# Kernel optimization log

Measured on AMD Instinct MI355X. Metric: run time of the kernel, lower is better.

## Reference

```python
import jax, jax.numpy as jnp
import numpy as np

N_NODES = 10000
DIM = 512
HEADS = 8
HEAD_DIM = DIM // HEADS  # 64
TOPK = 6
EPS = 1e-5
SLOPE = 0.01  # torch LeakyReLU default


def _layernorm(x, w, b):
    mu = x.mean(axis=-1, keepdims=True)
    var = ((x - mu) ** 2).mean(axis=-1, keepdims=True)
    return (x - mu) / jnp.sqrt(var + EPS) * w + b


def setup_inputs() -> dict:
    key = jax.random.key(0)
    ks = jax.random.split(key, 8)

    def w(k, shape):
        return jax.random.normal(k, shape, dtype=jnp.float32) * 0.02

    return {
        "x": jax.random.normal(ks[0], (1, N_NODES, DIM), dtype=jnp.float32),
        "fc1_w": w(ks[1], (DIM, DIM)), "fc1_b": jnp.zeros((DIM,), jnp.float32),
        "wh_w": w(ks[2], (DIM, DIM)), "wh_b": jnp.zeros((DIM,), jnp.float32),
        "wt_w": w(ks[3], (DIM, DIM)), "wt_b": jnp.zeros((DIM,), jnp.float32),
        "q_w": w(ks[4], (DIM, DIM)), "q_b": jnp.zeros((DIM,), jnp.float32),
        "kv_w": w(ks[5], (2 * DIM, DIM)), "kv_b": jnp.zeros((2 * DIM,), jnp.float32),
        "lin_w": w(ks[6], (DIM, DIM)), "lin_b": jnp.zeros((DIM,), jnp.float32),
        "norm_w": jnp.ones((DIM,), jnp.float32),
        "norm_b": jnp.zeros((DIM,), jnp.float32),
    }


def reference(x, fc1_w, fc1_b, wh_w, wh_b, wt_w, wt_b, q_w, q_b,
              kv_w, kv_b, lin_w, lin_b, norm_w, norm_b):
    # x: [1, N, DIM]
    n = x.shape[1]
    scale = HEAD_DIM ** -0.5

    x_input = x
    h = jax.nn.leaky_relu(x @ fc1_w.T + fc1_b, SLOPE)
    h = (h + h.mean(axis=1, keepdims=True)) * 0.5

    e_h = h @ wh_w.T + wh_b            # [1, N, DIM]
    e_t = h @ wt_w.T + wt_b            # [1, N, DIM]

    # dense graph-construction scores + per-row top-k neighbors
    logits = (e_h * scale) @ jnp.swapaxes(e_t, -2, -1)   # [1, N, N]
    _, topk_idx = jax.lax.top_k(logits, TOPK)            # [1, N, TOPK]

    # prototype node = most frequent tail index (torch unique+counts+argsort, top=1)
    counts = jnp.bincount(topk_idx.reshape(-1), length=n)
    top_node = jnp.argmax(counts)

    ins_top = jnp.take(x_input, top_node[None], axis=1)  # [1, 1, DIM]
    q_feat = jnp.take(h, top_node[None], axis=1)[0, 0]   # [DIM]

    # gather k=TOPK neighbor tail embeddings per node
    nb = e_t[0][topk_idx[0]]                              # [N, TOPK, DIM]

    q_heads = (q_feat @ q_w.T + q_b).reshape(HEADS, HEAD_DIM) * scale
    kv = (nb @ kv_w.T + kv_b).reshape(n, TOPK, 2, HEADS, HEAD_DIM)
    k_, v_ = kv[:, :, 0], kv[:, :, 1]                     # [N, TOPK, H, HD]

    attn = jnp.einsum('hd,nehd->nhe', q_heads, k_)        # [N, H, TOPK]
    attn = jax.nn.softmax(attn, axis=-1)
    out = jnp.einsum('nhe,nehd->nhd', attn, v_).reshape(n, DIM)

    e_nh = _layernorm(out, norm_w, norm_b)[None]          # [1, N, DIM]

    s = _layernorm(e_h + e_nh, norm_w, norm_b)
    s = jax.nn.leaky_relu(s @ lin_w.T + lin_b, SLOPE)     # dropout = identity (eval)
    embedding = s + x_input
    return embedding, ins_top
```

## Files before the change

kernel.cpp:

```cpp
#include <hip/hip_runtime.h>
#include <hip/hip_bf16.h>
#include <math.h>

#define N_NODES 10000
#define DIM 512
#define TOPK 6
#define NCHUNK 10
#define CHUNK 1024
#define NL 4
#define NCK 8
#define NC2 16
#define SLOPE 0.01
#define LN_EPS 1e-5f

typedef short bf16x8 __attribute__((ext_vector_type(8)));
typedef float f32x4 __attribute__((ext_vector_type(4)));
typedef double f64x4 __attribute__((ext_vector_type(4)));

__device__ __forceinline__ unsigned pack_key(float v, int idx)
{
    unsigned b = __float_as_uint(v);
    unsigned m = b ^ ((unsigned)((int)b >> 31) | 0x80000000u);
    return (m & 0xFFFFC000u) | (16383u - (unsigned)idx);
}

template <int D>
__device__ __forceinline__ void insert_u(unsigned (&k)[D], unsigned nk)
{
    if (nk > k[D - 1]) {
        k[D - 1] = nk;
#pragma unroll
        for (int s = D - 1; s > 0; s--) {
            unsigned hi = max(k[s], k[s - 1]);
            unsigned lo = min(k[s], k[s - 1]);
            k[s - 1] = hi; k[s] = lo;
        }
    }
}

__device__ __forceinline__ void gload16(const void* g, void* l)
{
    __builtin_amdgcn_global_load_lds(
        (const __attribute__((address_space(1))) void*)g,
        (__attribute__((address_space(3))) void*)l, 16, 0, 0);
}

__global__ __launch_bounds__(256) void colsum_part64(
    const double* __restrict__ h, double* __restrict__ part, int n, int nb)
{
    int b = blockIdx.x;
    int rows_per = (n + nb - 1) / nb;
    int r0 = b * rows_per, r1 = min(n, r0 + rows_per);
    int t = threadIdx.x;
    double s0 = 0.0, s1 = 0.0;
    for (int i = r0; i < r1; i++) {
        s0 += h[(size_t)i * DIM + t];
        s1 += h[(size_t)i * DIM + t + 256];
    }
    part[b * DIM + t] = s0;
    part[b * DIM + t + 256] = s1;
}

__global__ void colmean64(const double* __restrict__ part, double* __restrict__ mean,
                          int nb, int n)
{
    int j = blockIdx.x * blockDim.x + threadIdx.x;
    if (j < DIM) {
        double s = 0.0;
        for (int b = 0; b < nb; b++) s += part[b * DIM + j];
        mean[j] = s / (double)n;
    }
}

__global__ void cast_wb(const float* __restrict__ in1, short* __restrict__ o1, int n1,
                        const float* __restrict__ in2, short* __restrict__ o2)
{
    int i = (blockIdx.x * blockDim.x + threadIdx.x) * 4;
    const float* in = (i < n1) ? in1 + i : in2 + (i - n1);
    short* o = (i < n1) ? o1 + i : o2 + (i - n1);
    float4 f = *(const float4*)in;
    __hip_bfloat16 b0 = __float2bfloat16(f.x), b1 = __float2bfloat16(f.y);
    __hip_bfloat16 b2 = __float2bfloat16(f.z), b3 = __float2bfloat16(f.w);
    *(short4*)o = make_short4(*(short*)&b0, *(short*)&b1, *(short*)&b2, *(short*)&b3);
}

template <int POST, bool AF32, bool MIX, bool CASTF, bool CASTB>
__global__ __launch_bounds__(256, 4) void mfma_gemm_f64(
    const void* __restrict__ Av, const float* __restrict__ W,
    const float* __restrict__ bias, const double* __restrict__ mn,
    double* __restrict__ C, float* __restrict__ of, short* __restrict__ ob,
    int n, int K, int M)
{
    __shared__ double As[64][18];
    __shared__ double Bs[128][18];
    const int t = threadIdx.x, lane = t & 63, wid = t >> 6;
    const int lx = lane & 15, q = lane >> 4;
    const int wr = (wid >> 1) * 32, wc = (wid & 1) * 64;
    const int i0 = blockIdx.x * 64, j0 = blockIdx.y * 128;

    f64x4 acc[2][4];
#pragma unroll
    for (int a = 0; a < 2; a++)
#pragma unroll
        for (int b = 0; b < 4; b++) acc[a][b] = (f64x4)0.0;

    const int arow = t >> 2, askq = (t & 3) * 4;
    int gi = i0 + arow; if (gi >= n) gi = n - 1;
    const float*  af32 = (const float*)Av + (size_t)gi * K + askq;
    const double* af64 = (const double*)Av + (size_t)gi * K + askq;
    const int brow = t >> 1, bskq = (t & 1) * 8;
    const float* wrow = W + (size_t)(j0 + brow) * K + bskq;

    float4 wv0 = *(const float4*)(wrow);
    float4 wv1 = *(const float4*)(wrow + 4);
    float4 av;
    double2 a0v, a1v;
    if (AF32) av = *(const float4*)(af32);
    else { a0v = *(const double2*)(af64); a1v = *(const double2*)(af64 + 2); }

    for (int k0 = 0; k0 < K; k0 += 16) {
        __syncthreads();
        double m0 = 0, m1 = 0, m2 = 0, m3 = 0;
        if (MIX) {
            double2 mv0 = *(const double2*)(mn + k0 + askq);
            double2 mv1 = *(const double2*)(mn + k0 + askq + 2);
            m0 = mv0.x; m1 = mv0.y; m2 = mv1.x; m3 = mv1.y;
        }
        if (AF32) {
            As[arow][askq]     = (double)av.x; As[arow][askq + 1] = (double)av.y;
            As[arow][askq + 2] = (double)av.z; As[arow][askq + 3] = (double)av.w;
        } else if (MIX) {
            As[arow][askq]     = (a0v.x + m0) * 0.5; As[arow][askq + 1] = (a0v.y + m1) * 0.5;
            As[arow][askq + 2] = (a1v.x + m2) * 0.5; As[arow][askq + 3] = (a1v.y + m3) * 0.5;
        } else {
            As[arow][askq]     = a0v.x; As[arow][askq + 1] = a0v.y;
            As[arow][askq + 2] = a1v.x; As[arow][askq + 3] = a1v.y;
        }
        Bs[brow][bskq]     = (double)wv0.x; Bs[brow][bskq + 1] = (double)wv0.y;
        Bs[brow][bskq + 2] = (double)wv0.z; Bs[brow][bskq + 3] = (double)wv0.w;
        Bs[brow][bskq + 4] = (double)wv1.x; Bs[brow][bskq + 5] = (double)wv1.y;
        Bs[brow][bskq + 6] = (double)wv1.z; Bs[brow][bskq + 7] = (double)wv1.w;
        if (k0 + 16 < K) {
            wv0 = *(const float4*)(wrow + k0 + 16);
            wv1 = *(const float4*)(wrow + k0 + 20);
            if (AF32) av = *(const float4*)(af32 + k0 + 16);
            else { a0v = *(const double2*)(af64 + k0 + 16);
                   a1v = *(const double2*)(af64 + k0 + 18); }
        }
        __syncthreads();

#pragma unroll
        for (int ks = 0; ks < 4; ks++) {
            double a0 = As[wr + lx][ks * 4 + q];
            double a1 = As[wr + 16 + lx][ks * 4 + q];
#pragma unroll
            for (int cf = 0; cf < 4; cf++) {
                double b = Bs[wc + cf * 16 + lx][ks * 4 + q];
                acc[0][cf] = __builtin_amdgcn_mfma_f64_16x16x4f64(a0, b, acc[0][cf], 0, 0, 0);
                acc[1][cf] = __builtin_amdgcn_mfma_f64_16x16x4f64(a1, b, acc[1][cf], 0, 0, 0);
            }
        }
    }

#pragma unroll
    for (int rf = 0; rf < 2; rf++)
#pragma unroll
        for (int cf = 0; cf < 4; cf++)
#pragma unroll
            for (int reg = 0; reg < 4; reg++) {
                int gi2 = i0 + wr + rf * 16 + q * 4 + reg;
                int gj2 = j0 + wc + cf * 16 + lx;
                if (gi2 < n) {
                    double v = acc[rf][cf][reg] + (double)bias[gj2];
                    if (POST == 1) v = (v >= 0.0) ? v : v * SLOPE;
                    size_t idx = (size_t)gi2 * M + gj2;
                    C[idx] = v;
                    if (CASTF || CASTB) {
                        float f = (float)v;
                        if (CASTF) of[idx] = f;
                        if (CASTB) {
                            __hip_bfloat16 bb = __float2bfloat16(f);
                            ob[idx] = *reinterpret_cast<short*>(&bb);
                        }
                    }
                }
            }
}

__global__ __launch_bounds__(256, 3) void logits_topk_mfma(
    const short* __restrict__ eh, const short* __restrict__ et,
    unsigned* __restrict__ pk, int n)
{
    __shared__ short As[2][4096];
    __shared__ short Bs[2][4096];
    const int t = threadIdx.x;
    const int lane = t & 63, wid = t >> 6;
    const int lx = lane & 15, q = lane >> 4;

    int id = blockIdx.x, bx, chunk;
    if (id < 632) { chunk = id & 7; bx = id >> 3; }
    else { int r = id - 632; chunk = 8 + (r & 1); bx = r >> 1; }
    const int i0 = bx * 128;
    const int wbase = wid * 32;

    const int jlo = chunk * CHUNK;
    const int jhi = min(n, jlo + CHUNK);
    const int nj = (jhi - jlo + 127) >> 7;
    const int np = nj * 16;

    const int sslot = (t & 3) ^ ((t >> 3) & 3);
    const short* aP[2];
    const short* bP[2];
#pragma unroll
    for (int is = 0; is < 2; is++) {
        int row = is * 64 + (t >> 2);
        int ra = i0 + row; if (ra >= n) ra = n - 1;
        aP[is] = eh + (size_t)ra * DIM + sslot * 8;
    }
    const int slotq = (q ^ ((lx >> 1) & 3)) * 8;
    const int aOff = (wbase + lx) * 32 + slotq;
    const int bOff = lx * 32 + slotq;

    unsigned keys[8][NL];
#pragma unroll
    for (int r = 0; r < 8; r++)
#pragma unroll
        for (int s = 0; s < NL; s++) keys[r][s] = 0u;

    f32x4 acc[2][8];
#pragma unroll
    for (int rf = 0; rf < 2; rf++)
#pragma unroll
        for (int cf = 0; cf < 8; cf++) acc[rf][cf] = (f32x4)0.f;

    auto STAGE = [&](int buf, int ph) {
        int kk = ph & 15;
        if (kk == 0) {
            int j0 = jlo + (ph >> 4) * 128;
#pragma unroll
            for (int is = 0; is < 2; is++) {
                int row = is * 64 + (t >> 2);
                int rb = j0 + row; if (rb >= n) rb = n - 1;
                bP[is] = et + (size_t)rb * DIM + sslot * 8;
            }
        }
        int ko = kk * 32;
#pragma unroll
        for (int is = 0; is < 2; is++) {
            gload16(aP[is] + ko, &As[buf][is * 2048 + wid * 512]);
            gload16(bP[is] + ko, &Bs[buf][is * 2048 + wid * 512]);
        }
    };

    STAGE(0, 0);
    for (int p = 0; p < np; ++p) {
        __builtin_amdgcn_sched_barrier(0);
        __builtin_amdgcn_s_barrier();
        __builtin_amdgcn_sched_barrier(0);
        if (p + 1 < np) {
            STAGE((p + 1) & 1, p + 1);
            asm volatile("s_waitcnt vmcnt(4)" ::: "memory");
        } else {
            asm volatile("s_waitcnt vmcnt(0)" ::: "memory");
        }
        __builtin_amdgcn_sched_barrier(0);
        __builtin_amdgcn_s_barrier();
        __builtin_amdgcn_sched_barrier(0);

        const short* Ab = As[p & 1];
        const short* Bb = Bs[p & 1];
        bf16x8 a0 = *(const bf16x8*)(Ab + aOff);
        bf16x8 a1 = *(const bf16x8*)(Ab + aOff + 512);
#pragma unroll
        for (int cf = 0; cf < 8; cf++) {
            bf16x8 bw = *(const bf16x8*)(Bb + bOff + cf * 512);
            acc[0][cf] = __builtin_amdgcn_mfma_f32_16x16x32_bf16(
                a0, bw, acc[0][cf], 0, 0, 0);
            acc[1][cf] = __builtin_amdgcn_mfma_f32_16x16x32_bf16(
                a1, bw, acc[1][cf], 0, 0, 0);
        }

        if ((p & 15) == 15) {
            int j0 = jlo + (p >> 4) * 128;
#pragma unroll
            for (int rf = 0; rf < 2; rf++)
#pragma unroll
                for (int cf = 0; cf < 8; cf++) {
                    int gj = j0 + cf * 16 + lx;
                    if (gj < n) {
#pragma unroll
                        for (int reg = 0; reg < 4; reg++)
                            insert_u<NL>(keys[rf * 4 + reg],
                                         pack_key(acc[rf][cf][reg], gj));
                    }
                    acc[rf][cf] = (f32x4)0.f;
                }
        }
    }

#pragma unroll
    for (int rr = 0; rr < 8; rr++) {
        unsigned mk[NCK];
#pragma unroll
        for (int s = 0; s < NL; s++) mk[s] = keys[rr][s];
#pragma unroll
        for (int s = NL; s < NCK; s++) mk[s] = 0u;
        for (int m = 1; m < 16; m <<= 1) {
            unsigned sv[NCK];
#pragma unroll
            for (int s = 0; s < NCK; s++) sv[s] = mk[s];
#pragma unroll
            for (int s = 0; s < NCK; s++) {
                unsigned ov = (unsigned)__shfl_xor((int)sv[s], m);
                insert_u<NCK>(mk, ov);
            }
        }
        if (lx == 0) {
            int rf = rr >> 2, reg = rr & 3;
            int grow = i0 + wbase + rf * 16 + q * 4 + reg;
            if (grow < n) {
#pragma unroll
                for (int s = 0; s < NCK; s++)
                    pk[((size_t)chunk * N_NODES + grow) * NCK + s] = mk[s];
            }
        }
    }
}

template <int POST>
__global__ __launch_bounds__(256, 3) void mfma_gemm_bf16(
    const short* __restrict__ A, const short* __restrict__ W,
    const float* __restrict__ bias, const float* __restrict__ res,
    float* __restrict__ C, int n, int M)
{
    __shared__ short As[2][8192];
    __shared__ short Bs[2][8192];
    const int t = threadIdx.x;
    const int lane = t & 63, wid = t >> 6;
    const int lx = lane & 15, q = lane >> 4;
    const int lx7 = lane & 7;
    const int i0 = blockIdx.x * 128;
    const int j0 = blockIdx.y * 128;
    const int wbase = wid * 32;
    const int srl = lane >> 3;
    const int swz = (lane & 7) ^ srl;

    const short* aP[4];
    const short* bP[4];
#pragma unroll
    for (int is = 0; is < 4; is++) {
        int ra = i0 + is * 32 + wid * 8 + srl; if (ra >= n) ra = n - 1;
        aP[is] = A + (size_t)ra * DIM + swz * 8;
        int rb = j0 + is * 32 + wid * 8 + srl;
        bP[is] = W + (size_t)rb * DIM + swz * 8;
    }
    int aIdx[2], bIdx[2];
#pragma unroll
    for (int ks = 0; ks < 2; ks++) {
        int kap = (ks * 4 + q) ^ lx7;
        aIdx[ks] = (wbase + lx) * 64 + kap * 8;
        bIdx[ks] = lx * 64 + kap * 8;
    }

    f32x4 acc[2][8];
#pragma unroll
    for (int rf = 0; rf < 2; rf++)
#pragma unroll
        for (int cf = 0; cf < 8; cf++) acc[rf][cf] = (f32x4)0.f;

    auto STAGE = [&](int buf, int kk) {
        int ko = kk * 64;
        short* ab = &As[buf][wid * 512];
        short* bb = &Bs[buf][wid * 512];
#pragma unroll
        for (int is = 0; is < 4; is++) {
            gload16(aP[is] + ko, ab + is * 2048);
            gload16(bP[is] + ko, bb + is * 2048);
        }
    };

    STAGE(0, 0);
    for (int p = 0; p < 8; ++p) {
        __builtin_amdgcn_sched_barrier(0);
        __builtin_amdgcn_s_barrier();
        __builtin_amdgcn_sched_barrier(0);
        if (p + 1 < 8) {
            STAGE((p + 1) & 1, p + 1);
            asm volatile("s_waitcnt vmcnt(8)" ::: "memory");
        } else {
            asm volatile("s_waitcnt vmcnt(0)" ::: "memory");
        }
        __builtin_amdgcn_sched_barrier(0);
        __builtin_amdgcn_s_barrier();
        __builtin_amdgcn_sched_barrier(0);

        const short* Ab = As[p & 1];
        const short* Bb = Bs[p & 1];
#pragma unroll
        for (int ks = 0; ks < 2; ks++) {
            bf16x8 a0 = *(const bf16x8*)(Ab + aIdx[ks]);
            bf16x8 a1 = *(const bf16x8*)(Ab + aIdx[ks] + 1024);
#pragma unroll
            for (int cf = 0; cf < 8; cf++) {
                bf16x8 bw = *(const bf16x8*)(Bb + bIdx[ks] + cf * 1024);
                acc[0][cf] = __builtin_amdgcn_mfma_f32_16x16x32_bf16(
                    a0, bw, acc[0][cf], 0, 0, 0);
                acc[1][cf] = __builtin_amdgcn_mfma_f32_16x16x32_bf16(
                    a1, bw, acc[1][cf], 0, 0, 0);
            }
        }
    }

#pragma unroll
    for (int rf = 0; rf < 2; rf++)
#pragma unroll
        for (int cf = 0; cf < 8; cf++)
#pragma unroll
            for (int reg = 0; reg < 4; reg++) {
                int gi = i0 + wbase + rf * 16 + q * 4 + reg;
                int gj = j0 + cf * 16 + lx;
                if (gi < n) {
                    float v = acc[rf][cf][reg] + bias[gj];
                    if (POST >= 1) v = (v >= 0.f) ? v : v * SLOPE;
                    if (POST == 2) v += res[(size_t)gi * M + gj];
                    C[(size_t)gi * M + gj] = v;
                }
            }
}

__global__ void merge_chunks16(const unsigned* __restrict__ pk,
                               int* __restrict__ cand, int n)
{
    int row = blockIdx.x * blockDim.x + threadIdx.x;
    if (row >= n) return;
    unsigned bk[NC2];
#pragma unroll
    for (int s = 0; s < NC2; s++) bk[s] = 0u;
    for (int c = 0; c < NCHUNK; c++) {
#pragma unroll
        for (int s = 0; s < NCK; s++)
            insert_u<NC2>(bk, pk[((size_t)c * n + row) * NCK + s]);
    }
#pragma unroll
    for (int s = 0; s < NC2; s++)
        cand[row * NC2 + s] = 16383 - (int)(bk[s] & 16383u);
}

__global__ __launch_bounds__(256) void refine16(
    const double* __restrict__ ehd, const double* __restrict__ etd,
    const int* __restrict__ cand, int* __restrict__ tki,
    int* __restrict__ counts, int n)
{
    int row = blockIdx.x * 4 + (threadIdx.x >> 6);
    if (row >= n) return;
    int lane = threadIdx.x & 63;
    int c = lane >> 2, sub = lane & 3;
    int j = cand[row * NC2 + c];
    const double* er = ehd + (size_t)row * DIM;
    const double* tr = etd + (size_t)j * DIM;
    double s = 0.0;
#pragma unroll 8
    for (int k = sub; k < DIM; k += 4) s += er[k] * tr[k];
    s += __shfl_down(s, 2);
    s += __shfl_down(s, 1);
    double mine = __shfl(s, lane & ~3);
    int rank = 0;
#pragma unroll
    for (int m = 0; m < NC2; m++) {
        double vm = __shfl(s, m * 4);
        int jm = __shfl(j, m * 4);
        bool better = (vm > mine) || (vm == mine && jm < j);
        rank += better ? 1 : 0;
    }
    if (sub == 0 && rank < TOPK) {
        tki[row * TOPK + rank] = j;
        atomicAdd(&counts[j], 1);
    }
}

__global__ __launch_bounds__(1024) void argmax_kernel(
    const int* __restrict__ counts, int n, const float* __restrict__ x,
    int* __restrict__ topn, float* __restrict__ out_ins)
{
    __shared__ unsigned long long red[1024];
    int t = threadIdx.x;
    unsigned long long best = 0;
    for (int j = t; j < n; j += 1024) {
        unsigned long long key =
            ((unsigned long long)(unsigned)counts[j] << 32) | (unsigned)(n - 1 - j);
        if (key > best) best = key;
    }
    red[t] = best;
    __syncthreads();
    for (int s = 512; s > 0; s >>= 1) {
        if (t < s && red[t + s] > red[t]) red[t] = red[t + s];
        __syncthreads();
    }
    int tn = n - 1 - (int)(red[0] & 0xffffffffu);
    if (t == 0) *topn = tn;
    if (t < DIM) out_ins[t] = x[(size_t)tn * DIM + t];
}

__global__ __launch_bounds__(512) void qheads_kernel(
    const double* __restrict__ h2d, const double* __restrict__ mn,
    const int* __restrict__ topn, const float* __restrict__ qw,
    const float* __restrict__ qb, float* __restrict__ qh)
{
    __shared__ float qf[DIM];
    int t = threadIdx.x;
    int tn = *topn;
    qf[t] = (float)((h2d[(size_t)tn * DIM + t] + mn[t]) * 0.5);
    __syncthreads();
    int w = t >> 6, lane = t & 63;
    int jrow = blockIdx.x * 8 + w;
    float s = 0.f;
    for (int k = lane; k < DIM; k += 64) s += qf[k] * qw[(size_t)jrow * DIM + k];
#pragma unroll
    for (int m = 32; m > 0; m >>= 1) s += __shfl_down(s, m);
    if (lane == 0) qh[jrow] = (s + qb[jrow]) * 0.125f;
}

__global__ __launch_bounds__(512) void scores_kernel(
    const float* __restrict__ E, const float* __restrict__ qh, float* __restrict__ sc)
{
    int i = blockIdx.x;
    int t = threadIdx.x, w = t >> 6, lane = t & 63;
    float v = qh[t] * E[(size_t)i * 1024 + t];
#pragma unroll
    for (int m = 32; m > 0; m >>= 1) v += __shfl_down(v, m);
    if (lane == 0) sc[i * 8 + w] = v;
}

__global__ __launch_bounds__(512) void attn_ln_kernel(
    const float* __restrict__ E, const float* __restrict__ sc,
    const int* __restrict__ tki, const float* __restrict__ eh,
    const float* __restrict__ nw, const float* __restrict__ nbias,
    short* __restrict__ sprb, int n)
{
    __shared__ int nb[TOPK];
    __shared__ float red[16];
    __shared__ float stats[2];
    const int i = blockIdx.x;
    const int t = threadIdx.x;
    const int h = t >> 6, lane = t & 63;
    if (t < TOPK) nb[t] = tki[i * TOPK + t];
    __syncthreads();

    float myse = 0.f;
    if (lane < TOPK) myse = sc[(size_t)nb[lane] * 8 + h];
    float se[TOPK];
#pragma unroll
    for (int e = 0; e < TOPK; e++) se[e] = __shfl(myse, e);
    float mx = se[0];
#pragma unroll
    for (int e = 1; e < TOPK; e++) mx = fmaxf(mx, se[e]);
    float wsum = 0.f, w[TOPK];
#pragma unroll
    for (int e = 0; e < TOPK; e++) { w[e] = expf(se[e] - mx); wsum += w[e]; }
    float inv = 1.f / wsum;

    float o = 0.f;
#pragma unroll
    for (int e = 0; e < TOPK; e++) o += w[e] * E[(size_t)nb[e] * 1024 + 512 + t];
    o *= inv;

    float s1 = o, s2 = o * o;
#pragma unroll
    for (int m = 32; m > 0; m >>= 1) { s1 += __shfl_down(s1, m); s2 += __shfl_down(s2, m); }
    if (lane == 0) { red[h] = s1; red[h + 8] = s2; }
    __syncthreads();
    if (t == 0) {
        float a = 0.f, b = 0.f;
#pragma unroll
        for (int k = 0; k < 8; k++) { a += red[k]; b += red[k + 8]; }
        float mu = a * (1.f / 512.f);
        float var = b * (1.f / 512.f) - mu * mu;
        stats[0] = mu; stats[1] = rsqrtf(var + LN_EPS);
    }
    __syncthreads();
    float enh = (o - stats[0]) * stats[1] * nw[t] + nbias[t];
    float t2 = eh[(size_t)i * DIM + t] + enh;
    __syncthreads();

    s1 = t2; s2 = t2 * t2;
#pragma unroll
    for (int m = 32; m > 0; m >>= 1) { s1 += __shfl_down(s1, m); s2 += __shfl_down(s2, m); }
    if (lane == 0) { red[h] = s1; red[h + 8] = s2; }
    __syncthreads();
    if (t == 0) {
        float a = 0.f, b = 0.f;
#pragma unroll
        for (int k = 0; k < 8; k++) { a += red[k]; b += red[k + 8]; }
        float mu = a * (1.f / 512.f);
        float var = b * (1.f / 512.f) - mu * mu;
        stats[0] = mu; stats[1] = rsqrtf(var + LN_EPS);
    }
    __syncthreads();
    float sv = (t2 - stats[0]) * stats[1] * nw[t] + nbias[t];
    __hip_bfloat16 bb = __float2bfloat16(sv);
    sprb[(size_t)i * DIM + t] = *reinterpret_cast<short*>(&bb);
}

extern "C" void kernel_launch(void* const* d_in, const int* in_sizes, int n_in,
                              void* d_out, int out_size, void* d_ws, size_t ws_size,
                              hipStream_t stream)
{
    const float* x     = (const float*)d_in[0];
    const float* fc1_w = (const float*)d_in[1];
    const float* fc1_b = (const float*)d_in[2];
    const float* wh_w  = (const float*)d_in[3];
    const float* wh_b  = (const float*)d_in[4];
    const float* wt_w  = (const float*)d_in[5];
    const float* wt_b  = (const float*)d_in[6];
    const float* q_w   = (const float*)d_in[7];
    const float* q_b   = (const float*)d_in[8];
    const float* kv_w  = (const float*)d_in[9];
    const float* kv_b  = (const float*)d_in[10];
    const float* lin_w = (const float*)d_in[11];
    const float* lin_b = (const float*)d_in[12];
    const float* nw    = (const float*)d_in[13];
    const float* nbias = (const float*)d_in[14];
    float* out = (float*)d_out;

    const int n = N_NODES;
    size_t off = 0;
    auto take = [&](size_t bytes) -> void* {
        void* p = (void*)((char*)d_ws + off);
        off += (bytes + 255) & ~(size_t)255;
        return p;
    };
    double* h2d  = (double*)take((size_t)n * DIM * 8);
    double* ehd  = (double*)take((size_t)n * DIM * 8);
    double* etd  = (double*)take((size_t)n * DIM * 8);
    float*  ehf  = (float*)take((size_t)n * DIM * 4);
    short*  ehb  = (short*)take((size_t)n * DIM * 2);
    short*  etb  = (short*)take((size_t)n * DIM * 2);
    short*  sprb = (short*)take((size_t)n * DIM * 2);
    unsigned* pk = (unsigned*)take((size_t)NCHUNK * n * NCK * 4);
    int*    cand = (int*)take((size_t)n * NC2 * 4);
    int*    tki  = (int*)take((size_t)n * TOPK * 4);
    int*    counts = (int*)take((size_t)n * 4);
    int*    topn = (int*)take(256);
    float*  qh   = (float*)take(DIM * 4);
    float*  sc   = (float*)take((size_t)n * 8 * 4);
    double* part = (double*)take((size_t)160 * DIM * 8);
    double* mean = (double*)take(DIM * 8);
    short*  kvwb = (short*)take((size_t)1024 * DIM * 2);
    short*  linwb = (short*)take((size_t)512 * DIM * 2);
    float* E = (float*)h2d;

    hipMemsetAsync(counts, 0, n * sizeof(int), stream);

    dim3 b256(256);
    const int RB64 = (n + 63) / 64;
    const int RB2  = (n + 127) / 128;

    mfma_gemm_f64<1, true, false, false, false><<<dim3(RB64, 4), b256, 0, stream>>>(
        x, fc1_w, fc1_b, nullptr, h2d, nullptr, nullptr, n, DIM, DIM);
    colsum_part64<<<dim3(160), b256, 0, stream>>>(h2d, part, n, 160);
    colmean64<<<dim3(2), b256, 0, stream>>>(part, mean, 160, n);
    mfma_gemm_f64<0, false, true, true, true><<<dim3(RB64, 4), b256, 0, stream>>>(
        h2d, wh_w, wh_b, mean, ehd, ehf, ehb, n, DIM, DIM);
    mfma_gemm_f64<0, false, true, false, true><<<dim3(RB64, 4), b256, 0, stream>>>(
        h2d, wt_w, wt_b, mean, etd, nullptr, etb, n, DIM, DIM);
    cast_wb<<<dim3((1536 * DIM) / 1024), b256, 0, stream>>>(
        kv_w, kvwb, 1024 * DIM, lin_w, linwb);

    logits_topk_mfma<<<dim3(632 + 2 * RB2), b256, 0, stream>>>(ehb, etb, pk, n);
    merge_chunks16<<<dim3((n + 255) / 256), b256, 0, stream>>>(pk, cand, n);
    refine16<<<dim3((n + 3) / 4), b256, 0, stream>>>(ehd, etd, cand, tki, counts, n);

    argmax_kernel<<<dim3(1), dim3(1024), 0, stream>>>(counts, n, x, topn,
                                                      out + (size_t)n * DIM);
    qheads_kernel<<<dim3(64), dim3(512), 0, stream>>>(h2d, mean, topn, q_w, q_b, qh);
    mfma_gemm_bf16<0><<<dim3(RB2, 8), b256, 0, stream>>>(
        etb, kvwb, kv_b, nullptr, E, n, 1024);
    scores_kernel<<<dim3(n), dim3(512), 0, stream>>>(E, qh, sc);
    attn_ln_kernel<<<dim3(n), dim3(512), 0, stream>>>(E, sc, tki, ehf, nw, nbias, sprb, n);
    mfma_gemm_bf16<2><<<dim3(RB2, 4), b256, 0, stream>>>(
        sprb, linwb, lin_b, x, out, n, 512);
}
```

Before: 842.7 us.

## Merge eh/et GEMMs into one launch and remap blocks for XCD-aware scheduling

```diff
diff --git a/kernel.cpp b/kernel.cpp
--- a/kernel.cpp
+++ b/kernel.cpp
@@ -12,6 +12,7 @@
 #define NC2 16
 #define SLOPE 0.01
 #define LN_EPS 1e-5f
+#define NB_COL 320
 
 typedef short bf16x8 __attribute__((ext_vector_type(8)));
 typedef float f32x4 __attribute__((ext_vector_type(4)));
@@ -84,19 +85,23 @@
     *(short4*)o = make_short4(*(short*)&b0, *(short*)&b1, *(short*)&b2, *(short*)&b3);
 }
 
-template <int POST, bool AF32, bool MIX, bool CASTF, bool CASTB>
-__global__ __launch_bounds__(256, 4) void mfma_gemm_f64(
-    const void* __restrict__ Av, const float* __restrict__ W,
-    const float* __restrict__ bias, const double* __restrict__ mn,
-    double* __restrict__ C, float* __restrict__ of, short* __restrict__ ob,
-    int n, int K, int M)
-{
+__global__ __launch_bounds__(256, 4) void gemm_fc1(
+    const float* __restrict__ X, const float* __restrict__ W,
+    const float* __restrict__ bias, double* __restrict__ C, int n)
+{
+    const int K = DIM, M = DIM;
+    const int id = blockIdx.x;
+    const int c = id & 7, kk2 = id >> 3;
+    const int y = kk2 & 3, mm = kk2 >> 2;
+    const int bx = c + 8 * mm;
+    if (bx >= (n + 63) / 64) return;
+
     __shared__ double As[64][18];
     __shared__ double Bs[128][18];
     const int t = threadIdx.x, lane = t & 63, wid = t >> 6;
     const int lx = lane & 15, q = lane >> 4;
     const int wr = (wid >> 1) * 32, wc = (wid & 1) * 64;
-    const int i0 = blockIdx.x * 64, j0 = blockIdx.y * 128;
+    const int i0 = bx * 64, j0 = y * 128;
 
     f64x4 acc[2][4];
 #pragma unroll
@@ -106,36 +111,18 @@
 
     const int arow = t >> 2, askq = (t & 3) * 4;
     int gi = i0 + arow; if (gi >= n) gi = n - 1;
-    const float*  af32 = (const float*)Av + (size_t)gi * K + askq;
-    const double* af64 = (const double*)Av + (size_t)gi * K + askq;
+    const float* af32 = X + (size_t)gi * K + askq;
     const int brow = t >> 1, bskq = (t & 1) * 8;
     const float* wrow = W + (size_t)(j0 + brow) * K + bskq;
 
     float4 wv0 = *(const float4*)(wrow);
     float4 wv1 = *(const float4*)(wrow + 4);
-    float4 av;
-    double2 a0v, a1v;
-    if (AF32) av = *(const float4*)(af32);
-    else { a0v = *(const double2*)(af64); a1v = *(const double2*)(af64 + 2); }
+    float4 av = *(const float4*)(af32);
 
     for (int k0 = 0; k0 < K; k0 += 16) {
         __syncthreads();
-        double m0 = 0, m1 = 0, m2 = 0, m3 = 0;
-        if (MIX) {
-            double2 mv0 = *(const double2*)(mn + k0 + askq);
-            double2 mv1 = *(const double2*)(mn + k0 + askq + 2);
-            m0 = mv0.x; m1 = mv0.y; m2 = mv1.x; m3 = mv1.y;
-        }
-        if (AF32) {
-            As[arow][askq]     = (double)av.x; As[arow][askq + 1] = (double)av.y;
-            As[arow][askq + 2] = (double)av.z; As[arow][askq + 3] = (double)av.w;
-        } else if (MIX) {
-            As[arow][askq]     = (a0v.x + m0) * 0.5; As[arow][askq + 1] = (a0v.y + m1) * 0.5;
-            As[arow][askq + 2] = (a1v.x + m2) * 0.5; As[arow][askq + 3] = (a1v.y + m3) * 0.5;
-        } else {
-            As[arow][askq]     = a0v.x; As[arow][askq + 1] = a0v.y;
-            As[arow][askq + 2] = a1v.x; As[arow][askq + 3] = a1v.y;
-        }
+        As[arow][askq]     = (double)av.x; As[arow][askq + 1] = (double)av.y;
+        As[arow][askq + 2] = (double)av.z; As[arow][askq + 3] = (double)av.w;
         Bs[brow][bskq]     = (double)wv0.x; Bs[brow][bskq + 1] = (double)wv0.y;
         Bs[brow][bskq + 2] = (double)wv0.z; Bs[brow][bskq + 3] = (double)wv0.w;
         Bs[brow][bskq + 4] = (double)wv1.x; Bs[brow][bskq + 5] = (double)wv1.y;
@@ -143,9 +130,7 @@
         if (k0 + 16 < K) {
             wv0 = *(const float4*)(wrow + k0 + 16);
             wv1 = *(const float4*)(wrow + k0 + 20);
-            if (AF32) av = *(const float4*)(af32 + k0 + 16);
-            else { a0v = *(const double2*)(af64 + k0 + 16);
-                   a1v = *(const double2*)(af64 + k0 + 18); }
+            av  = *(const float4*)(af32 + k0 + 16);
         }
         __syncthreads();
 
@@ -172,17 +157,102 @@
                 int gj2 = j0 + wc + cf * 16 + lx;
                 if (gi2 < n) {
                     double v = acc[rf][cf][reg] + (double)bias[gj2];
-                    if (POST == 1) v = (v >= 0.0) ? v : v * SLOPE;
+                    v = (v >= 0.0) ? v : v * SLOPE;
+                    C[(size_t)gi2 * M + gj2] = v;
+                }
+            }
+}
+
+__global__ __launch_bounds__(256, 4) void gemm_ehet(
+    const double* __restrict__ H, const float* __restrict__ whw,
+    const float* __restrict__ whb, const float* __restrict__ wtw,
+    const float* __restrict__ wtb, const double* __restrict__ mn,
+    double* __restrict__ ehd, float* __restrict__ ehf, short* __restrict__ ehb2,
+    double* __restrict__ etd, short* __restrict__ etb2, int n)
+{
+    const int K = DIM, M = DIM;
+    const int id = blockIdx.x;
+    const int c = id & 7, kk2 = id >> 3;
+    const int y = kk2 & 7, mm = kk2 >> 3;
+    const int bx = c + 8 * mm;
+    if (bx >= (n + 63) / 64) return;
+    const bool isH = (y < 4);
+    const float* W    = isH ? whw : wtw;
+    const float* bias = isH ? whb : wtb;
+    double* C  = isH ? ehd : etd;
+    short*  ob = isH ? ehb2 : etb2;
+
+    __shared__ double As[64][18];
+    __shared__ double Bs[128][18];
+    const int t = threadIdx.x, lane = t & 63, wid = t >> 6;
+    const int lx = lane & 15, q = lane >> 4;
+    const int wr = (wid >> 1) * 32, wc = (wid & 1) * 64;
+    const int i0 = bx * 64, j0 = (y & 3) * 128;
+
+    f64x4 acc[2][4];
+#pragma unroll
+    for (int a = 0; a < 2; a++)
+#pragma unroll
+        for (int b = 0; b < 4; b++) acc[a][b] = (f64x4)0.0;
+
+    const int arow = t >> 2, askq = (t & 3) * 4;
+    int gi = i0 + arow; if (gi >= n) gi = n - 1;
+    const double* af64 = H + (size_t)gi * K + askq;
+    const int brow = t >> 1, bskq = (t & 1) * 8;
+    const float* wrow = W + (size_t)(j0 + brow) * K + bskq;
+
+    float4 wv0 = *(const float4*)(wrow);
+    float4 wv1 = *(const float4*)(wrow + 4);
+    double2 a0v = *(const double2*)(af64);
+    double2 a1v = *(const double2*)(af64 + 2);
+
+    for (int k0 = 0; k0 < K; k0 += 16) {
+        __syncthreads();
+        double2 mv0 = *(const double2*)(mn + k0 + askq);
+        double2 mv1 = *(const double2*)(mn + k0 + askq + 2);
+        As[arow][askq]     = (a0v.x + mv0.x) * 0.5; As[arow][askq + 1] = (a0v.y + mv0.y) * 0.5;
+        As[arow][askq + 2] = (a1v.x + mv1.x) * 0.5; As[arow][askq + 3] = (a1v.y + mv1.y) * 0.5;
+        Bs[brow][bskq]     = (double)wv0.x; Bs[brow][bskq + 1] = (double)wv0.y;
+        Bs[brow][bskq + 2] = (double)wv0.z; Bs[brow][bskq + 3] = (double)wv0.w;
+        Bs[brow][bskq + 4] = (double)wv1.x; Bs[brow][bskq + 5] = (double)wv1.y;
+        Bs[brow][bskq + 6] = (double)wv1.z; Bs[brow][bskq + 7] = (double)wv1.w;
+        if (k0 + 16 < K) {
+            wv0 = *(const float4*)(wrow + k0 + 16);
+            wv1 = *(const float4*)(wrow + k0 + 20);
+            a0v = *(const double2*)(af64 + k0 + 16);
+            a1v = *(const double2*)(af64 + k0 + 18);
+        }
+        __syncthreads();
+
+#pragma unroll
+        for (int ks = 0; ks < 4; ks++) {
+            double a0 = As[wr + lx][ks * 4 + q];
+            double a1 = As[wr + 16 + lx][ks * 4 + q];
+#pragma unroll
+            for (int cf = 0; cf < 4; cf++) {
+                double b = Bs[wc + cf * 16 + lx][ks * 4 + q];
+                acc[0][cf] = __builtin_amdgcn_mfma_f64_16x16x4f64(a0, b, acc[0][cf], 0, 0, 0);
+                acc[1][cf] = __builtin_amdgcn_mfma_f64_16x16x4f64(a1, b, acc[1][cf], 0, 0, 0);
+            }
+        }
+    }
+
+#pragma unroll
+    for (int rf = 0; rf < 2; rf++)
+#pragma unroll
+        for (int cf = 0; cf < 4; cf++)
+#pragma unroll
+            for (int reg = 0; reg < 4; reg++) {
+                int gi2 = i0 + wr + rf * 16 + q * 4 + reg;
+                int gj2 = j0 + wc + cf * 16 + lx;
+                if (gi2 < n) {
+                    double v = acc[rf][cf][reg] + (double)bias[gj2];
                     size_t idx = (size_t)gi2 * M + gj2;
                     C[idx] = v;
-                    if (CASTF || CASTB) {
-                        float f = (float)v;
-                        if (CASTF) of[idx] = f;
-                        if (CASTB) {
-                            __hip_bfloat16 bb = __float2bfloat16(f);
-                            ob[idx] = *reinterpret_cast<short*>(&bb);
-                        }
-                    }
+                    float f = (float)v;
+                    if (isH) ehf[idx] = f;
+                    __hip_bfloat16 bb = __float2bfloat16(f);
+                    ob[idx] = *reinterpret_cast<short*>(&bb);
                 }
             }
 }
@@ -327,20 +397,26 @@
     }
 }
 
-template <int POST>
+template <int POST, int NY, int LY>
 __global__ __launch_bounds__(256, 3) void mfma_gemm_bf16(
     const short* __restrict__ A, const short* __restrict__ W,
     const float* __restrict__ bias, const float* __restrict__ res,
     float* __restrict__ C, int n, int M)
 {
+    const int id = blockIdx.x;
+    const int c = id & 7, kk2 = id >> 3;
+    const int y = kk2 & (NY - 1), mm = kk2 >> LY;
+    const int bxx = c + 8 * mm;
+    if (bxx >= (n + 127) / 128) return;
+
     __shared__ short As[2][8192];
     __shared__ short Bs[2][8192];
     const int t = threadIdx.x;
     const int lane = t & 63, wid = t >> 6;
     const int lx = lane & 15, q = lane >> 4;
     const int lx7 = lane & 7;
-    const int i0 = blockIdx.x * 128;
-    const int j0 = blockIdx.y * 128;
+    const int i0 = bxx * 128;
+    const int j0 = y * 128;
     const int wbase = wid * 32;
     const int srl = lane >> 3;
     const int swz = (lane & 7) ^ srl;
@@ -643,7 +719,7 @@
     int*    topn = (int*)take(256);
     float*  qh   = (float*)take(DIM * 4);
     float*  sc   = (float*)take((size_t)n * 8 * 4);
-    double* part = (double*)take((size_t)160 * DIM * 8);
+    double* part = (double*)take((size_t)NB_COL * DIM * 8);
     double* mean = (double*)take(DIM * 8);
     short*  kvwb = (short*)take((size_t)1024 * DIM * 2);
     short*  linwb = (short*)take((size_t)512 * DIM * 2);
@@ -652,17 +728,13 @@
     hipMemsetAsync(counts, 0, n * sizeof(int), stream);
 
     dim3 b256(256);
-    const int RB64 = (n + 63) / 64;
-    const int RB2  = (n + 127) / 128;
-
-    mfma_gemm_f64<1, true, false, false, false><<<dim3(RB64, 4), b256, 0, stream>>>(
-        x, fc1_w, fc1_b, nullptr, h2d, nullptr, nullptr, n, DIM, DIM);
-    colsum_part64<<<dim3(160), b256, 0, stream>>>(h2d, part, n, 160);
-    colmean64<<<dim3(2), b256, 0, stream>>>(part, mean, 160, n);
-    mfma_gemm_f64<0, false, true, true, true><<<dim3(RB64, 4), b256, 0, stream>>>(
-        h2d, wh_w, wh_b, mean, ehd, ehf, ehb, n, DIM, DIM);
-    mfma_gemm_f64<0, false, true, false, true><<<dim3(RB64, 4), b256, 0, stream>>>(
-        h2d, wt_w, wt_b, mean, etd, nullptr, etb, n, DIM, DIM);
+    const int RB2 = (n + 127) / 128;
+
+    gemm_fc1<<<dim3(640), b256, 0, stream>>>(x, fc1_w, fc1_b, h2d, n);
+    colsum_part64<<<dim3(NB_COL), b256, 0, stream>>>(h2d, part, n, NB_COL);
+    colmean64<<<dim3(2), b256, 0, stream>>>(part, mean, NB_COL, n);
+    gemm_ehet<<<dim3(1280), b256, 0, stream>>>(
+        h2d, wh_w, wh_b, wt_w, wt_b, mean, ehd, ehf, ehb, etd, etb, n);
     cast_wb<<<dim3((1536 * DIM) / 1024), b256, 0, stream>>>(
         kv_w, kvwb, 1024 * DIM, lin_w, linwb);
 
@@ -673,10 +745,10 @@
     argmax_kernel<<<dim3(1), dim3(1024), 0, stream>>>(counts, n, x, topn,
                                                       out + (size_t)n * DIM);
     qheads_kernel<<<dim3(64), dim3(512), 0, stream>>>(h2d, mean, topn, q_w, q_b, qh);
-    mfma_gemm_bf16<0><<<dim3(RB2, 8), b256, 0, stream>>>(
+    mfma_gemm_bf16<0, 8, 3><<<dim3(640), b256, 0, stream>>>(
         etb, kvwb, kv_b, nullptr, E, n, 1024);
     scores_kernel<<<dim3(n), dim3(512), 0, stream>>>(E, qh, sc);
     attn_ln_kernel<<<dim3(n), dim3(512), 0, stream>>>(E, sc, tki, ehf, nw, nbias, sprb, n);
-    mfma_gemm_bf16<2><<<dim3(RB2, 4), b256, 0, stream>>>(
+    mfma_gemm_bf16<2, 4, 2><<<dim3(320), b256, 0, stream>>>(
         sprb, linwb, lin_b, x, out, n, 512);
 }
```

After: 829.3 us. Within noise of the previous version (-1.6%).
